# Kernel optimization log

Hardware: AMD Instinct MI355X
Metric: run time of the kernel (lower is better)

The kernel has to match this reference:

```python
import jax, jax.numpy as jnp
import numpy as np

BN_EPS = 1e-5


def conv1d(x, w, stride, pad):
    # x: [N, C, T], w: [O, I, K]
    return jax.lax.conv_general_dilated(
        x, w, window_strides=(stride,), padding=[(pad, pad)],
        dimension_numbers=('NCH', 'OIH', 'NCH'))


def setup_inputs() -> dict:
    key = jax.random.key(0)
    ks = jax.random.split(key, 10)
    B, Cin, T = 32, 80, 1024
    C, D, M = 768, 64, 512
    s = 0.02
    inp = {
        'mels': jax.random.normal(ks[0], (B, Cin, T), jnp.float32),
        'w1': jax.random.normal(ks[1], (C, Cin, 3), jnp.float32) * s,
        'w2': jax.random.normal(ks[2], (C, C, 3), jnp.float32) * s,
        'w3': jax.random.normal(ks[3], (C, C, 4), jnp.float32) * s,
        'w4': jax.random.normal(ks[4], (C, C, 3), jnp.float32) * s,
        'w5': jax.random.normal(ks[5], (C, C, 3), jnp.float32) * s,
        'w6': jax.random.normal(ks[6], (D, C, 1), jnp.float32) * s,
        'b6': jnp.zeros((D,), jnp.float32),
        'bn_gamma': jnp.ones((5, C), jnp.float32),
        'bn_beta': jnp.zeros((5, C), jnp.float32),
        'bn_mean': jnp.zeros((5, C), jnp.float32),
        'bn_var': jnp.ones((5, C), jnp.float32),
        'embedding': jax.random.uniform(ks[7], (M, D), jnp.float32,
                                        minval=-1.0 / 512, maxval=1.0 / 512),
    }
    return inp


def reference(mels, w1, w2, w3, w4, w5, w6, b6,
              bn_gamma, bn_beta, bn_mean, bn_var, embedding):
    def block(x, w, stride, pad, i):
        x = conv1d(x, w, stride, pad)
        inv = bn_gamma[i] / jnp.sqrt(bn_var[i] + BN_EPS)
        x = x * inv[None, :, None] + (bn_beta[i] - bn_mean[i] * inv)[None, :, None]
        return jax.nn.relu(x)

    z = block(mels, w1, 1, 0, 0)   # [B, C, 1022]
    z = block(z, w2, 1, 1, 1)
    z = block(z, w3, 2, 1, 2)      # [B, C, 511]
    z = block(z, w4, 1, 1, 3)
    z = block(z, w5, 1, 1, 4)
    z = conv1d(z, w6, 1, 0) + b6[None, :, None]  # [B, D, 511]
    z = jnp.transpose(z, (0, 2, 1))              # [B, T', D]

    B, Tp, D = z.shape
    M = embedding.shape[0]
    x_flat = jax.lax.stop_gradient(z).reshape(-1, D)  # [N, D]
    dists = (jnp.sum(embedding ** 2, axis=1)[None, :]
             + jnp.sum(x_flat ** 2, axis=1, keepdims=True)
             - 2.0 * x_flat @ embedding.T)
    idx = jnp.argmin(dists, axis=-1)                  # [N]
    quantized = embedding[idx].reshape(B, Tp, D)
    loss = 0.25 * jnp.mean((z - jax.lax.stop_gradient(quantized)) ** 2)
    q_st = z + jax.lax.stop_gradient(quantized - z)   # straight-through
    counts = jnp.zeros((M,), jnp.float32).at[idx].add(1.0)
    avg_probs = counts / idx.shape[0]
    perplexity = jnp.exp(-jnp.sum(avg_probs * jnp.log(avg_probs + 1e-10)))
    return (q_st, loss, perplexity)
```

## Files before the change

### kernel.cpp

```cpp
#include <hip/hip_runtime.h>
#include <cstddef>
#include <cstdint>

#define BN_EPS 1e-5f

typedef _Float16 half8 __attribute__((ext_vector_type(8)));
typedef float f32x4v __attribute__((ext_vector_type(4)));

__device__ __forceinline__ unsigned split_pack(float v) {
    _Float16 h = (_Float16)v;
    float r = (v - (float)h) * 2048.0f;
    _Float16 l = (_Float16)r;
    unsigned short hu = __builtin_bit_cast(unsigned short, h);
    unsigned short lu = __builtin_bit_cast(unsigned short, l);
    return (unsigned)hu | ((unsigned)lu << 16);
}

__global__ __launch_bounds__(256)
void prep_w(const float* __restrict__ w, unsigned* __restrict__ wp,
            int Cin, int KW, int CIPAD)
{
    int id = blockIdx.x * 256 + threadIdx.x;
    int total = KW * 768 * CIPAD;
    if (id >= total) return;
    int cip = id % CIPAD;
    int co  = (id / CIPAD) % 768;
    int kw  = id / (CIPAD * 768);
    float v = 0.0f;
    if (cip < Cin) v = w[((size_t)co * Cin + cip) * KW + kw];
    wp[id] = split_pack(v * 256.0f);
}

__global__ __launch_bounds__(256)
void prep_mels(const float* __restrict__ mels, unsigned* __restrict__ mt)
{
    int id = blockIdx.x * 256 + threadIdx.x;
    if (id >= 32 * 1032 * 96) return;
    int c = id % 96;
    int t = (id / 96) % 1032;
    int b = id / (96 * 1032);
    float v = 0.0f;
    if (c < 80 && t < 1024) v = mels[((size_t)b * 80 + c) * 1024 + t];
    mt[id] = split_pack(v * 16.0f);
}

template<int KW, int S, int P, int CIPAD, int TIN, int TSIN, int TOUT, int TSOUT, int EPI>
__global__ __launch_bounds__(512, 4)
void conv_mfma(const unsigned* __restrict__ Xin, const unsigned* __restrict__ Wp,
               const float* __restrict__ gamma, const float* __restrict__ beta,
               const float* __restrict__ mean, const float* __restrict__ var,
               unsigned* __restrict__ Uout, float* __restrict__ Fout)
{
    constexpr int NCI = CIPAD / 32;
    constexpr int NC  = KW * NCI;
    __shared__ unsigned smem[16896];
    _Float16* sm = (_Float16*)smem;

    const int gx = gridDim.x, gy = gridDim.y;
    const int nwg  = gx * gy * (int)gridDim.z;
    const int flat = blockIdx.x + gx * (blockIdx.y + gy * blockIdx.z);
    const int swz  = (flat & 7) * (nwg >> 3) + (flat >> 3);
    const int cox  = swz % gx;
    const int rem  = swz / gx;
    const int ty   = rem % gy;
    const int b    = rem / gy;

    const int co0 = cox * 128;
    const int t0  = ty * 128;
    const int tid = threadIdx.x;
    const int lane = tid & 63, wv = tid >> 6;
    const int quad = lane >> 4, l16 = lane & 15;
    const int wm = (wv & 1) * 64;
    const int wn = (wv >> 1) * 32;

    f32x4v accH[4][2] = {};
    f32x4v accX[4][2] = {};

    const int ab   = tid >> 8;
    const int r2   = tid & 255;
    const int srow = r2 >> 1;
    const int sh   = r2 & 1;
    const unsigned* __restrict__ xb = Xin + (size_t)b * TSIN * CIPAD;

    uint4 rT[4];

    auto loadT = [&](int c) {
        const int kw  = c / NCI;
        const int ci0 = (c % NCI) * 32;
        if (ab == 0) {
            const unsigned* pA = Wp + (size_t)(kw * 768 + co0 + srow) * CIPAD + ci0;
            rT[0] = *(const uint4*)(pA + sh * 8);
            rT[1] = *(const uint4*)(pA + sh * 8 + 4);
            rT[2] = *(const uint4*)(pA + (sh + 2) * 8);
            rT[3] = *(const uint4*)(pA + (sh + 2) * 8 + 4);
        } else {
            const int tp = (t0 + srow) * S + kw - P;
            rT[0] = rT[1] = rT[2] = rT[3] = make_uint4(0, 0, 0, 0);
            if ((unsigned)tp < (unsigned)TIN) {
                const unsigned* pB = xb + (size_t)tp * CIPAD + ci0;
                rT[0] = *(const uint4*)(pB + sh * 8);
                rT[1] = *(const uint4*)(pB + sh * 8 + 4);
                rT[2] = *(const uint4*)(pB + (sh + 2) * 8);
                rT[3] = *(const uint4*)(pB + (sh + 2) * 8 + 4);
            }
        }
    };

    auto splitHL = [](uint4 a, uint4 b2, uint4& h, uint4& l) {
        h.x = (a.x & 0xffffu) | (a.y << 16);
        h.y = (a.z & 0xffffu) | (a.w << 16);
        h.z = (b2.x & 0xffffu) | (b2.y << 16);
        h.w = (b2.z & 0xffffu) | (b2.w << 16);
        l.x = (a.x >> 16) | (a.y & 0xffff0000u);
        l.y = (a.z >> 16) | (a.w & 0xffff0000u);
        l.z = (b2.x >> 16) | (b2.y & 0xffff0000u);
        l.w = (b2.z >> 16) | (b2.w & 0xffff0000u);
    };

    auto storeT = [&](int pbuf) {
        const int b0 = pbuf * 16384 + ab * 8192;
        const int u1 = (((srow >> 4) * 4 + sh) * 16 + (srow & 15)) * 8;
        const int u2 = u1 + 256;
        uint4 h, l;
        splitHL(rT[0], rT[1], h, l);
        *(uint4*)(sm + b0 + 0    + u1) = h;
        *(uint4*)(sm + b0 + 4096 + u1) = l;
        splitHL(rT[2], rT[3], h, l);
        *(uint4*)(sm + b0 + 0    + u2) = h;
        *(uint4*)(sm + b0 + 4096 + u2) = l;
    };

    loadT(0);
    storeT(0);
    if (NC > 1) loadT(1);
    __syncthreads();

    int p = 0;
    for (int c = 0; c < NC; ++c) {
        const int base = p * 16384;
        if (c + 1 < NC) storeT(p ^ 1);
        if (c + 2 < NC) loadT(c + 2);

        half8 bh[2], bl[2];
#pragma unroll
        for (int nt = 0; nt < 2; ++nt) {
            int gn = (wv >> 1) * 2 + nt;
            int u = ((gn * 4 + quad) * 16 + l16) * 8;
            bh[nt] = *(const half8*)(sm + base + 8192  + u);
            bl[nt] = *(const half8*)(sm + base + 12288 + u);
        }
#pragma unroll
        for (int mt = 0; mt < 4; ++mt) {
            int gm = (wv & 1) * 4 + mt;
            int u = ((gm * 4 + quad) * 16 + l16) * 8;
            half8 ah = *(const half8*)(sm + base + 0    + u);
            half8 al = *(const half8*)(sm + base + 4096 + u);
#pragma unroll
            for (int nt = 0; nt < 2; ++nt) {
                accH[mt][nt] = __builtin_amdgcn_mfma_f32_16x16x32_f16(ah, bh[nt], accH[mt][nt], 0, 0, 0);
                accX[mt][nt] = __builtin_amdgcn_mfma_f32_16x16x32_f16(ah, bl[nt], accX[mt][nt], 0, 0, 0);
                accX[mt][nt] = __builtin_amdgcn_mfma_f32_16x16x32_f16(al, bh[nt], accX[mt][nt], 0, 0, 0);
            }
        }
        __syncthreads();
        p ^= 1;
    }

    if constexpr (EPI == 0) {
        unsigned* bb = smem;
#pragma unroll
        for (int mt = 0; mt < 4; ++mt) {
#pragma unroll
            for (int r = 0; r < 4; ++r) {
                int mloc = wm + mt * 16 + quad * 4 + r;
                int co = co0 + mloc;
                float iv = gamma[co] / sqrtf(var[co] + BN_EPS);
                float sh2 = beta[co] - mean[co] * iv;
#pragma unroll
                for (int nt = 0; nt < 2; ++nt) {
                    float vf = (accH[mt][nt][r] + accX[mt][nt][r] * (1.0f / 2048.0f)) * (1.0f / 4096.0f);
                    float y = fmaf(vf, iv, sh2);
                    y = y > 0.0f ? y : 0.0f;
                    bb[(wn + nt * 16 + l16) * 132 + mloc] = split_pack(y * 16.0f);
                }
            }
        }
        __syncthreads();
        int tl = tid >> 2, seg = tid & 3;
        int t = t0 + tl;
        if (t < TOUT) {
            uint4* dst = (uint4*)(Uout + ((size_t)b * TSOUT + t) * 768 + co0 + seg * 32);
            const uint4* src = (const uint4*)(bb + tl * 132 + seg * 32);
#pragma unroll
            for (int i = 0; i < 8; ++i) dst[i] = src[i];
        }
    } else {
#pragma unroll
        for (int mt = 0; mt < 4; ++mt) {
#pragma unroll
            for (int r = 0; r < 4; ++r) {
                int co = co0 + wm + mt * 16 + quad * 4 + r;
                float iv = gamma[co] / sqrtf(var[co] + BN_EPS);
                float sh2 = beta[co] - mean[co] * iv;
                float* op = Fout + ((size_t)b * 768 + co) * TOUT;
#pragma unroll
                for (int nt = 0; nt < 2; ++nt) {
                    int t = t0 + wn + nt * 16 + l16;
                    if (t < TOUT) {
                        float vf = (accH[mt][nt][r] + accX[mt][nt][r] * (1.0f / 2048.0f)) * (1.0f / 4096.0f);
                        float y = fmaf(vf, iv, sh2);
                        op[t] = y > 0.0f ? y : 0.0f;
                    }
                }
            }
        }
    }
}

constexpr int TM = 64, TN = 64, TK = 16;

__global__ __launch_bounds__(256)
void conv1x1_bias_T(const float* __restrict__ in, const float* __restrict__ w,
                    const float* __restrict__ bias, float* __restrict__ z,
                    int Cin, int T)
{
    const int b   = blockIdx.z;
    const int t0  = blockIdx.y * TN;
    const int tid = threadIdx.x;

    __shared__ float As[TK][TM + 4];
    __shared__ float Bs[TK][TN + 4];

    float acc[4][4] = {};

    const int m0 = (tid & 15) * 4;
    const int n0 = (tid >> 4) * 4;

    const float* __restrict__ inb = in + (size_t)b * Cin * T;

    const int a_m = tid >> 4;
    const int a_k = tid & 15;
    const int b_k = tid >> 6;
    const int b_n = tid & 63;

    for (int kc = 0; kc < Cin; kc += TK) {
        __syncthreads();
#pragma unroll
        for (int i = 0; i < 4; ++i) {
            int m = a_m + 16 * i;
            As[a_k][m] = w[(size_t)m * Cin + kc + a_k];
        }
#pragma unroll
        for (int i = 0; i < 4; ++i) {
            int kk = b_k + 4 * i;
            int ci = kc + kk;
            int t  = t0 + b_n;
            Bs[kk][b_n] = (t < T) ? inb[(size_t)ci * T + t] : 0.0f;
        }
        __syncthreads();
#pragma unroll
        for (int kk = 0; kk < TK; ++kk) {
            float4 av = *reinterpret_cast<const float4*>(&As[kk][m0]);
            float4 bv = *reinterpret_cast<const float4*>(&Bs[kk][n0]);
            float am[4] = {av.x, av.y, av.z, av.w};
            float bn[4] = {bv.x, bv.y, bv.z, bv.w};
#pragma unroll
            for (int mi = 0; mi < 4; ++mi)
#pragma unroll
                for (int nj = 0; nj < 4; ++nj)
                    acc[mi][nj] = fmaf(am[mi], bn[nj], acc[mi][nj]);
        }
    }

    float4 bb = *reinterpret_cast<const float4*>(&bias[m0]);
    float bs[4] = {bb.x, bb.y, bb.z, bb.w};
#pragma unroll
    for (int nj = 0; nj < 4; ++nj) {
        int t = t0 + n0 + nj;
        if (t < T) {
            float4 v;
            v.x = acc[0][nj] + bs[0];
            v.y = acc[1][nj] + bs[1];
            v.z = acc[2][nj] + bs[2];
            v.w = acc[3][nj] + bs[3];
            *reinterpret_cast<float4*>(&z[((size_t)b * T + t) * 64 + m0]) = v;
        }
    }
}

__global__ __launch_bounds__(256)
void vq_e2(const float* __restrict__ emb, float* __restrict__ e2)
{
    int m = blockIdx.x * 256 + threadIdx.x;
    if (m < 512) {
        float s = 0.0f;
#pragma unroll
        for (int d = 0; d < 64; ++d) {
            float v = emb[(size_t)m * 64 + d];
            s = fmaf(v, v, s);
        }
        e2[m] = s;
    }
}

__global__ __launch_bounds__(64)
void vq_argmin(const float* __restrict__ z, const float* __restrict__ emb,
               const float* __restrict__ e2, int* __restrict__ idx,
               float* __restrict__ counts, int N)
{
    __shared__ float Es[64 * 64];
    const int tid = threadIdx.x;
    const int n   = blockIdx.x * 64 + tid;
    const bool act = n < N;

    float x[64];
    float x2 = 0.0f;
    if (act) {
        const float4* zp = reinterpret_cast<const float4*>(z + (size_t)n * 64);
#pragma unroll
        for (int i = 0; i < 16; ++i) {
            float4 v = zp[i];
            x[4 * i + 0] = v.x; x[4 * i + 1] = v.y;
            x[4 * i + 2] = v.z; x[4 * i + 3] = v.w;
        }
#pragma unroll
        for (int d = 0; d < 64; ++d) x2 = fmaf(x[d], x[d], x2);
    }

    float best = 3.4e38f;
    int   bi   = 0;
    for (int c = 0; c < 8; ++c) {
        __syncthreads();
        const float4* ep  = reinterpret_cast<const float4*>(emb + (size_t)c * 4096);
        float4*       esp = reinterpret_cast<float4*>(Es);
#pragma unroll
        for (int i = 0; i < 16; ++i) esp[tid + 64 * i] = ep[tid + 64 * i];
        __syncthreads();
        for (int r = 0; r < 64; ++r) {
            const float4* er = reinterpret_cast<const float4*>(&Es[r * 64]);
            float dot = 0.0f;
#pragma unroll
            for (int i = 0; i < 16; ++i) {
                float4 e4 = er[i];
                dot = fmaf(x[4 * i + 0], e4.x, dot);
                dot = fmaf(x[4 * i + 1], e4.y, dot);
                dot = fmaf(x[4 * i + 2], e4.z, dot);
                dot = fmaf(x[4 * i + 3], e4.w, dot);
            }
            float dist = (e2[c * 64 + r] + x2) - 2.0f * dot;
            if (dist < best) { best = dist; bi = c * 64 + r; }
        }
    }
    if (act) {
        idx[n] = bi;
        atomicAdd(&counts[bi], 1.0f);
    }
}

__global__ __launch_bounds__(256)
void vq_quant_loss(const float* __restrict__ z, const float* __restrict__ emb,
                   const int* __restrict__ idx, float* __restrict__ qout,
                   double* __restrict__ loss_sum, int Ntot)
{
    int g = blockIdx.x * 256 + threadIdx.x;
    float d2 = 0.0f;
    if (g < Ntot) {
        int n = g >> 6;
        int d = g & 63;
        float q  = emb[(size_t)idx[n] * 64 + d];
        float zv = z[g];
        qout[g] = zv + (q - zv);
        float diff = zv - q;
        d2 = diff * diff;
    }
#pragma unroll
    for (int o = 32; o > 0; o >>= 1) d2 += __shfl_down(d2, o);
    __shared__ float wsum[4];
    if ((threadIdx.x & 63) == 0) wsum[threadIdx.x >> 6] = d2;
    __syncthreads();
    if (threadIdx.x == 0)
        atomicAdd(loss_sum, (double)(wsum[0] + wsum[1] + wsum[2] + wsum[3]));
}

__global__ __launch_bounds__(512)
void vq_finalize(const float* __restrict__ counts, const double* __restrict__ loss_sum,
                 float* __restrict__ out, int Ntot, int Npts)
{
    int t = threadIdx.x;
    float c   = counts[t];
    float avg = c / (float)Npts;
    float term = avg * logf(avg + 1e-10f);
#pragma unroll
    for (int o = 32; o > 0; o >>= 1) term += __shfl_down(term, o);
    __shared__ float wsum[8];
    if ((t & 63) == 0) wsum[t >> 6] = term;
    __syncthreads();
    if (t == 0) {
        float s = 0.0f;
        for (int i = 0; i < 8; ++i) s += wsum[i];
        out[Ntot]     = 0.25f * (float)(loss_sum[0] / (double)Ntot);
        out[Ntot + 1] = expf(-s);
    }
}

extern "C" void kernel_launch(void* const* d_in, const int* in_sizes, int n_in,
                              void* d_out, int out_size, void* d_ws, size_t ws_size,
                              hipStream_t stream)
{
    const float* mels     = (const float*)d_in[0];
    const float* w1       = (const float*)d_in[1];
    const float* w2       = (const float*)d_in[2];
    const float* w3       = (const float*)d_in[3];
    const float* w4       = (const float*)d_in[4];
    const float* w5       = (const float*)d_in[5];
    const float* w6       = (const float*)d_in[6];
    const float* b6       = (const float*)d_in[7];
    const float* bn_gamma = (const float*)d_in[8];
    const float* bn_beta  = (const float*)d_in[9];
    const float* bn_mean  = (const float*)d_in[10];
    const float* bn_var   = (const float*)d_in[11];
    const float* emb      = (const float*)d_in[12];

    constexpr int B = 32, C = 768, D = 64, T2 = 511;

    char* ws = (char*)d_ws;
    unsigned* P1 = (unsigned*)ws;
    unsigned* P2 = (unsigned*)(ws + 100663296);
    unsigned* Wp = (unsigned*)(ws + 201326592);
    size_t misc  = 201326592 + 9437184;
    float*  counts = (float*)(ws + misc);
    double* lossp  = (double*)(ws + misc + 2048);
    float*  e2p    = (float*)(ws + misc + 2048 + 64);
    int*    idx    = (int*)(ws + misc + 2048 + 64 + 2048);

    unsigned* melsT = P2;
    float*    bufA  = (float*)P1;
    float*    z     = (float*)P2;

    hipMemsetAsync(ws + misc, 0, 2048 + 64, stream);

    vq_e2<<<dim3(2), 256, 0, stream>>>(emb, e2p);
    prep_mels<<<dim3((32 * 1032 * 96 + 255) / 256), 256, 0, stream>>>(mels, melsT);

    prep_w<<<dim3((3 * 768 * 96 + 255) / 256), 256, 0, stream>>>(w1, Wp, 80, 3, 96);
    conv_mfma<3, 1, 0, 96, 1032, 1032, 1022, 1024, 0><<<dim3(6, 8, B), 512, 0, stream>>>(
        melsT, Wp, bn_gamma + 0 * C, bn_beta + 0 * C, bn_mean + 0 * C, bn_var + 0 * C, P1, nullptr);
    prep_w<<<dim3((3 * 768 * 768 + 255) / 256), 256, 0, stream>>>(w2, Wp, 768, 3, 768);
    conv_mfma<3, 1, 1, 768, 1022, 1024, 1022, 1024, 0><<<dim3(6, 8, B), 512, 0, stream>>>(
        P1, Wp, bn_gamma + 1 * C, bn_beta + 1 * C, bn_mean + 1 * C, bn_var + 1 * C, P2, nullptr);
    prep_w<<<dim3((4 * 768 * 768 + 255) / 256), 256, 0, stream>>>(w3, Wp, 768, 4, 768);
    conv_mfma<4, 2, 1, 768, 1022, 1024, 511, 512, 0><<<dim3(6, 4, B), 512, 0, stream>>>(
        P2, Wp, bn_gamma + 2 * C, bn_beta + 2 * C, bn_mean + 2 * C, bn_var + 2 * C, P1, nullptr);
    prep_w<<<dim3((3 * 768 * 768 + 255) / 256), 256, 0, stream>>>(w4, Wp, 768, 3, 768);
    conv_mfma<3, 1, 1, 768, 511, 512, 511, 512, 0><<<dim3(6, 4, B), 512, 0, stream>>>(
        P1, Wp, bn_gamma + 3 * C, bn_beta + 3 * C, bn_mean + 3 * C, bn_var + 3 * C, P2, nullptr);
    prep_w<<<dim3((3 * 768 * 768 + 255) / 256), 256, 0, stream>>>(w5, Wp, 768, 3, 768);
    conv_mfma<3, 1, 1, 768, 511, 512, 511, 511, 1><<<dim3(6, 4, B), 512, 0, stream>>>(
        P2, Wp, bn_gamma + 4 * C, bn_beta + 4 * C, bn_mean + 4 * C, bn_var + 4 * C, nullptr, bufA);

    conv1x1_bias_T<<<dim3(1, 8, B), 256, 0, stream>>>(bufA, w6, b6, z, C, T2);

    const int Npts = B * T2;
    const int Ntot = Npts * D;
    vq_argmin<<<dim3((Npts + 63) / 64), 64, 0, stream>>>(z, emb, e2p, idx, counts, Npts);
    vq_quant_loss<<<dim3(Ntot / 256), 256, 0, stream>>>(z, emb, idx, (float*)d_out, lossp, Ntot);
    vq_finalize<<<dim3(1), 512, 0, stream>>>(counts, lossp, (float*)d_out, Ntot, Npts);
}
```

Measured before the change: 1.508 ms.

## Store split-fp16 activations and weights as separate hi/lo planes

Activations and weights are now stored as two separate fp16 planes (high and low parts) instead of interleaved 32-bit hi/lo pairs. The split into planes happens once in the producer kernel epilogues and prep kernels, so the conv main loop no longer repacks bits before each shared-memory store. This cuts ALU work and register pressure in the hot tile-load path. Global traffic stays the same, and the epilogue does slightly more work.

```diff
diff --git a/kernel.cpp b/kernel.cpp
--- a/kernel.cpp
+++ b/kernel.cpp
@@ -16,9 +16,20 @@
     return (unsigned)hu | ((unsigned)lu << 16);
 }
 
+__device__ __forceinline__ void splitHL(uint4 a, uint4 b2, uint4& h, uint4& l) {
+    h.x = (a.x & 0xffffu) | (a.y << 16);
+    h.y = (a.z & 0xffffu) | (a.w << 16);
+    h.z = (b2.x & 0xffffu) | (b2.y << 16);
+    h.w = (b2.z & 0xffffu) | (b2.w << 16);
+    l.x = (a.x >> 16) | (a.y & 0xffff0000u);
+    l.y = (a.z >> 16) | (a.w & 0xffff0000u);
+    l.z = (b2.x >> 16) | (b2.y & 0xffff0000u);
+    l.w = (b2.z >> 16) | (b2.w & 0xffff0000u);
+}
+
 __global__ __launch_bounds__(256)
-void prep_w(const float* __restrict__ w, unsigned* __restrict__ wp,
-            int Cin, int KW, int CIPAD)
+void prep_w(const float* __restrict__ w, unsigned short* __restrict__ wh,
+            unsigned short* __restrict__ wl, int Cin, int KW, int CIPAD)
 {
     int id = blockIdx.x * 256 + threadIdx.x;
     int total = KW * 768 * CIPAD;
@@ -28,11 +39,14 @@
     int kw  = id / (CIPAD * 768);
     float v = 0.0f;
     if (cip < Cin) v = w[((size_t)co * Cin + cip) * KW + kw];
-    wp[id] = split_pack(v * 256.0f);
+    unsigned pk = split_pack(v * 256.0f);
+    wh[id] = (unsigned short)pk;
+    wl[id] = (unsigned short)(pk >> 16);
 }
 
 __global__ __launch_bounds__(256)
-void prep_mels(const float* __restrict__ mels, unsigned* __restrict__ mt)
+void prep_mels(const float* __restrict__ mels, unsigned short* __restrict__ mh,
+               unsigned short* __restrict__ ml)
 {
     int id = blockIdx.x * 256 + threadIdx.x;
     if (id >= 32 * 1032 * 96) return;
@@ -41,15 +55,19 @@
     int b = id / (96 * 1032);
     float v = 0.0f;
     if (c < 80 && t < 1024) v = mels[((size_t)b * 80 + c) * 1024 + t];
-    mt[id] = split_pack(v * 16.0f);
+    unsigned pk = split_pack(v * 16.0f);
+    mh[id] = (unsigned short)pk;
+    ml[id] = (unsigned short)(pk >> 16);
 }
 
 template<int KW, int S, int P, int CIPAD, int TIN, int TSIN, int TOUT, int TSOUT, int EPI>
 __global__ __launch_bounds__(512, 4)
-void conv_mfma(const unsigned* __restrict__ Xin, const unsigned* __restrict__ Wp,
+void conv_mfma(const unsigned short* __restrict__ XH, const unsigned short* __restrict__ XL,
+               const unsigned short* __restrict__ WH, const unsigned short* __restrict__ WL,
                const float* __restrict__ gamma, const float* __restrict__ beta,
                const float* __restrict__ mean, const float* __restrict__ var,
-               unsigned* __restrict__ Uout, float* __restrict__ Fout)
+               unsigned short* __restrict__ OutH, unsigned short* __restrict__ OutL,
+               float* __restrict__ Fout)
 {
     constexpr int NCI = CIPAD / 32;
     constexpr int NC  = KW * NCI;
@@ -80,54 +98,41 @@
     const int r2   = tid & 255;
     const int srow = r2 >> 1;
     const int sh   = r2 & 1;
-    const unsigned* __restrict__ xb = Xin + (size_t)b * TSIN * CIPAD;
-
-    uint4 rT[4];
+    const unsigned short* __restrict__ xhb = XH + (size_t)b * TSIN * CIPAD;
+    const unsigned short* __restrict__ xlb = XL + (size_t)b * TSIN * CIPAD;
+
+    uint4 rH[2], rL[2];
 
     auto loadT = [&](int c) {
         const int kw  = c / NCI;
         const int ci0 = (c % NCI) * 32;
         if (ab == 0) {
-            const unsigned* pA = Wp + (size_t)(kw * 768 + co0 + srow) * CIPAD + ci0;
-            rT[0] = *(const uint4*)(pA + sh * 8);
-            rT[1] = *(const uint4*)(pA + sh * 8 + 4);
-            rT[2] = *(const uint4*)(pA + (sh + 2) * 8);
-            rT[3] = *(const uint4*)(pA + (sh + 2) * 8 + 4);
+            const size_t o = (size_t)(kw * 768 + co0 + srow) * CIPAD + ci0;
+            rH[0] = *(const uint4*)(WH + o + sh * 8);
+            rH[1] = *(const uint4*)(WH + o + (sh + 2) * 8);
+            rL[0] = *(const uint4*)(WL + o + sh * 8);
+            rL[1] = *(const uint4*)(WL + o + (sh + 2) * 8);
         } else {
             const int tp = (t0 + srow) * S + kw - P;
-            rT[0] = rT[1] = rT[2] = rT[3] = make_uint4(0, 0, 0, 0);
+            rH[0] = rH[1] = rL[0] = rL[1] = make_uint4(0, 0, 0, 0);
             if ((unsigned)tp < (unsigned)TIN) {
-                const unsigned* pB = xb + (size_t)tp * CIPAD + ci0;
-                rT[0] = *(const uint4*)(pB + sh * 8);
-                rT[1] = *(const uint4*)(pB + sh * 8 + 4);
-                rT[2] = *(const uint4*)(pB + (sh + 2) * 8);
-                rT[3] = *(const uint4*)(pB + (sh + 2) * 8 + 4);
-            }
-        }
-    };
-
-    auto splitHL = [](uint4 a, uint4 b2, uint4& h, uint4& l) {
-        h.x = (a.x & 0xffffu) | (a.y << 16);
-        h.y = (a.z & 0xffffu) | (a.w << 16);
-        h.z = (b2.x & 0xffffu) | (b2.y << 16);
-        h.w = (b2.z & 0xffffu) | (b2.w << 16);
-        l.x = (a.x >> 16) | (a.y & 0xffff0000u);
-        l.y = (a.z >> 16) | (a.w & 0xffff0000u);
-        l.z = (b2.x >> 16) | (b2.y & 0xffff0000u);
-        l.w = (b2.z >> 16) | (b2.w & 0xffff0000u);
+                const size_t o = (size_t)tp * CIPAD + ci0;
+                rH[0] = *(const uint4*)(xhb + o + sh * 8);
+                rH[1] = *(const uint4*)(xhb + o + (sh + 2) * 8);
+                rL[0] = *(const uint4*)(xlb + o + sh * 8);
+                rL[1] = *(const uint4*)(xlb + o + (sh + 2) * 8);
+            }
+        }
     };
 
     auto storeT = [&](int pbuf) {
         const int b0 = pbuf * 16384 + ab * 8192;
         const int u1 = (((srow >> 4) * 4 + sh) * 16 + (srow & 15)) * 8;
         const int u2 = u1 + 256;
-        uint4 h, l;
-        splitHL(rT[0], rT[1], h, l);
-        *(uint4*)(sm + b0 + 0    + u1) = h;
-        *(uint4*)(sm + b0 + 4096 + u1) = l;
-        splitHL(rT[2], rT[3], h, l);
-        *(uint4*)(sm + b0 + 0    + u2) = h;
-        *(uint4*)(sm + b0 + 4096 + u2) = l;
+        *(uint4*)(sm + b0 + 0    + u1) = rH[0];
+        *(uint4*)(sm + b0 + 4096 + u1) = rL[0];
+        *(uint4*)(sm + b0 + 0    + u2) = rH[1];
+        *(uint4*)(sm + b0 + 4096 + u2) = rL[1];
     };
 
     loadT(0);
@@ -189,10 +194,15 @@
         int tl = tid >> 2, seg = tid & 3;
         int t = t0 + tl;
         if (t < TOUT) {
-            uint4* dst = (uint4*)(Uout + ((size_t)b * TSOUT + t) * 768 + co0 + seg * 32);
             const uint4* src = (const uint4*)(bb + tl * 132 + seg * 32);
-#pragma unroll
-            for (int i = 0; i < 8; ++i) dst[i] = src[i];
+            size_t base2 = ((size_t)b * TSOUT + t) * 768 + co0 + seg * 32;
+#pragma unroll
+            for (int i = 0; i < 4; ++i) {
+                uint4 h, l;
+                splitHL(src[2 * i], src[2 * i + 1], h, l);
+                *(uint4*)(OutH + base2 + i * 8) = h;
+                *(uint4*)(OutL + base2 + i * 8) = l;
+            }
         }
     } else {
 #pragma unroll
@@ -424,39 +434,49 @@
     constexpr int B = 32, C = 768, D = 64, T2 = 511;
 
     char* ws = (char*)d_ws;
-    unsigned* P1 = (unsigned*)ws;
-    unsigned* P2 = (unsigned*)(ws + 100663296);
-    unsigned* Wp = (unsigned*)(ws + 201326592);
+    constexpr size_t ACT = (size_t)32 * 1024 * 768;
+    unsigned short* P1H = (unsigned short*)ws;
+    unsigned short* P1L = P1H + ACT;
+    unsigned short* P2H = (unsigned short*)(ws + 100663296);
+    unsigned short* P2L = P2H + ACT;
+    unsigned short* WHp = (unsigned short*)(ws + 201326592);
+    unsigned short* WLp = WHp + (size_t)4 * 768 * 768;
     size_t misc  = 201326592 + 9437184;
     float*  counts = (float*)(ws + misc);
     double* lossp  = (double*)(ws + misc + 2048);
     float*  e2p    = (float*)(ws + misc + 2048 + 64);
     int*    idx    = (int*)(ws + misc + 2048 + 64 + 2048);
 
-    unsigned* melsT = P2;
-    float*    bufA  = (float*)P1;
-    float*    z     = (float*)P2;
+    unsigned short* MH = P2H;
+    unsigned short* ML = P2L;
+    float* bufA = (float*)ws;
+    float* z    = (float*)(ws + 100663296);
 
     hipMemsetAsync(ws + misc, 0, 2048 + 64, stream);
 
     vq_e2<<<dim3(2), 256, 0, stream>>>(emb, e2p);
-    prep_mels<<<dim3((32 * 1032 * 96 + 255) / 256), 256, 0, stream>>>(mels, melsT);
-
-    prep_w<<<dim3((3 * 768 * 96 + 255) / 256), 256, 0, stream>>>(w1, Wp, 80, 3, 96);
+    prep_mels<<<dim3((32 * 1032 * 96 + 255) / 256), 256, 0, stream>>>(mels, MH, ML);
+
+    prep_w<<<dim3((3 * 768 * 96 + 255) / 256), 256, 0, stream>>>(w1, WHp, WLp, 80, 3, 96);
     conv_mfma<3, 1, 0, 96, 1032, 1032, 1022, 1024, 0><<<dim3(6, 8, B), 512, 0, stream>>>(
-        melsT, Wp, bn_gamma + 0 * C, bn_beta + 0 * C, bn_mean + 0 * C, bn_var + 0 * C, P1, nullptr);
-    prep_w<<<dim3((3 * 768 * 768 + 255) / 256), 256, 0, stream>>>(w2, Wp, 768, 3, 768);
+        MH, ML, WHp, WLp, bn_gamma + 0 * C, bn_beta + 0 * C, bn_mean + 0 * C, bn_var + 0 * C,
+        P1H, P1L, nullptr);
+    prep_w<<<dim3((3 * 768 * 768 + 255) / 256), 256, 0, stream>>>(w2, WHp, WLp, 768, 3, 768);
     conv_mfma<3, 1, 1, 768, 1022, 1024, 1022, 1024, 0><<<dim3(6, 8, B), 512, 0, stream>>>(
-        P1, Wp, bn_gamma + 1 * C, bn_beta + 1 * C, bn_mean + 1 * C, bn_var + 1 * C, P2, nullptr);
-    prep_w<<<dim3((4 * 768 * 768 + 255) / 256), 256, 0, stream>>>(w3, Wp, 768, 4, 768);
+        P1H, P1L, WHp, WLp, bn_gamma + 1 * C, bn_beta + 1 * C, bn_mean + 1 * C, bn_var + 1 * C,
+        P2H, P2L, nullptr);
+    prep_w<<<dim3((4 * 768 * 768 + 255) / 256), 256, 0, stream>>>(w3, WHp, WLp, 768, 4, 768);
     conv_mfma<4, 2, 1, 768, 1022, 1024, 511, 512, 0><<<dim3(6, 4, B), 512, 0, stream>>>(
-        P2, Wp, bn_gamma + 2 * C, bn_beta + 2 * C, bn_mean + 2 * C, bn_var + 2 * C, P1, nullptr);
-    prep_w<<<dim3((3 * 768 * 768 + 255) / 256), 256, 0, stream>>>(w4, Wp, 768, 3, 768);
+        P2H, P2L, WHp, WLp, bn_gamma + 2 * C, bn_beta + 2 * C, bn_mean + 2 * C, bn_var + 2 * C,
+        P1H, P1L, nullptr);
+    prep_w<<<dim3((3 * 768 * 768 + 255) / 256), 256, 0, stream>>>(w4, WHp, WLp, 768, 3, 768);
     conv_mfma<3, 1, 1, 768, 511, 512, 511, 512, 0><<<dim3(6, 4, B), 512, 0, stream>>>(
-        P1, Wp, bn_gamma + 3 * C, bn_beta + 3 * C, bn_mean + 3 * C, bn_var + 3 * C, P2, nullptr);
-    prep_w<<<dim3((3 * 768 * 768 + 255) / 256), 256, 0, stream>>>(w5, Wp, 768, 3, 768);
+        P1H, P1L, WHp, WLp, bn_gamma + 3 * C, bn_beta + 3 * C, bn_mean + 3 * C, bn_var + 3 * C,
+        P2H, P2L, nullptr);
+    prep_w<<<dim3((3 * 768 * 768 + 255) / 256), 256, 0, stream>>>(w5, WHp, WLp, 768, 3, 768);
     conv_mfma<3, 1, 1, 768, 511, 512, 511, 511, 1><<<dim3(6, 4, B), 512, 0, stream>>>(
-        P2, Wp, bn_gamma + 4 * C, bn_beta + 4 * C, bn_mean + 4 * C, bn_var + 4 * C, nullptr, bufA);
+        P2H, P2L, WHp, WLp, bn_gamma + 4 * C, bn_beta + 4 * C, bn_mean + 4 * C, bn_var + 4 * C,
+        nullptr, nullptr, bufA);
 
     conv1x1_bias_T<<<dim3(1, 8, B), 256, 0, stream>>>(bufA, w6, b6, z, C, T2);
 
```

Result: no change. 1.483 ms (-1.7%).
